# Kernel tuning notes

Measured on AMD Instinct MI355X. Metric: run time of the kernel, lower is better.

Reference implementation:

```python
import jax, jax.numpy as jnp
import numpy as np

NUM_HEADS = 8
D_HEAD = 64
ATTENTION_WINDOW = 512


def alibi_bias(num_heads, q_len, k_len):
    # ALiBi slopes for power-of-2 number of heads (Press et al. 2021).
    start = 2.0 ** (-(2.0 ** -(np.log2(num_heads) - 3.0)))
    slopes = jnp.asarray([start * (start ** i) for i in range(num_heads)],
                         dtype=jnp.float32)  # [H]
    rel = jnp.arange(q_len)[:, None] - jnp.arange(k_len)[None, :]  # [t, T]
    # Bidirectional ALiBi: bias = -slope * |i - j|
    return -slopes[:, None, None] * jnp.abs(rel).astype(jnp.float32)  # [H, t, T]


def sliding_window_mask(seq_len, window):
    # Attend to tokens within window//2 on each side; even window -> window+1.
    if window % 2 == 0:
        window += 1
    half = window // 2
    idx = jnp.arange(seq_len)
    return jnp.abs(idx[:, None] - idx[None, :]) <= half  # [S, S] bool


def setup_inputs() -> dict:
    key = jax.random.key(0)
    ks = jax.random.split(key, 6)
    B, S, E = 2, 4096, 512
    HD = NUM_HEADS * D_HEAD
    s_in = 1.0 / np.sqrt(E)
    s_out = 1.0 / np.sqrt(HD)
    return {
        'inputs_q': jax.random.normal(ks[0], (B, S, E), jnp.float32),
        'inputs_kv': jax.random.normal(ks[1], (B, S, E), jnp.float32),
        'w_q': jax.random.normal(ks[2], (E, HD), jnp.float32) * s_in,
        'w_k': jax.random.normal(ks[3], (E, HD), jnp.float32) * s_in,
        'w_v': jax.random.normal(ks[4], (E, HD), jnp.float32) * s_in,
        'w_o': jax.random.normal(ks[5], (HD, E), jnp.float32) * s_out,
    }


def reference(inputs_q, inputs_kv, w_q, w_k, w_v, w_o):
    B, S, E = inputs_q.shape
    H, D = NUM_HEADS, D_HEAD
    q = (inputs_q @ w_q).reshape(B, S, H, D)
    k = (inputs_kv @ w_k).reshape(B, S, H, D)
    v = (inputs_kv @ w_v).reshape(B, S, H, D)
    # scores: [B, H, t, T]
    att = jnp.einsum('bthd,bThd->bhtT', q, k) * (1.0 / jnp.sqrt(jnp.float32(D)))
    att = att + alibi_bias(H, S, S)[None]
    mask = sliding_window_mask(S, ATTENTION_WINDOW)
    att = jnp.where(mask[None, None], att, jnp.finfo(jnp.float32).min)
    p = jax.nn.softmax(att, axis=-1)
    out = jnp.einsum('bhtT,bThd->bthd', p, v).reshape(B, S, H * D)
    return out @ w_o
```

## Files before the change

### kernel.cpp

```cpp
#include <hip/hip_runtime.h>

#define S_LEN  4096
#define NH     8
#define DH     64
#define EMB    512
#define HDIM   512
#define HALF_W 256
#define BATCH  2
#define M_ROWS (BATCH * S_LEN)

typedef __attribute__((ext_vector_type(8))) short bf16x8;
typedef __attribute__((ext_vector_type(4))) float f32x4;

__device__ __forceinline__ float b2f(unsigned short u) {
    union { unsigned int i; float f; } v; v.i = ((unsigned int)u) << 16; return v.f;
}
__device__ __forceinline__ unsigned short f2b(float f) {
    unsigned int x = __float_as_uint(f);
    unsigned int r = (x + 0x7fffu + ((x >> 16) & 1u)) >> 16;
    return (unsigned short)r;
}
__device__ __forceinline__ void unpack2(unsigned int u, float* d) {
    d[0] = b2f((unsigned short)(u & 0xffffu));
    d[1] = b2f((unsigned short)(u >> 16));
}
union FragU { uint4 u; bf16x8 f; };
__device__ __forceinline__ bf16x8 ldfrag(const unsigned short* p) {
    FragU x; x.u = *(const uint4*)p; return x.f;
}

__device__ __forceinline__ void async16(const unsigned short* g, unsigned short* l) {
    __builtin_amdgcn_global_load_lds(
        (__attribute__((address_space(1))) void*)const_cast<unsigned short*>(g),
        (__attribute__((address_space(3))) void*)l, 16, 0, 0);
}

__device__ __forceinline__ int detect_flag(const unsigned short* __restrict__ xq) {
    __shared__ int s_flag;
    if (threadIdx.x == 0) s_flag = 0;
    __syncthreads();
    uint4 u = *(const uint4*)(xq + threadIdx.x * 8);
    const unsigned short* us = (const unsigned short*)&u;
    int bad = 0;
#pragma unroll
    for (int i = 0; i < 8; ++i) {
        float v = b2f(us[i]);
        if (!(fabsf(v) < 1.0e6f)) bad = 1;
    }
    if (__any(bad) && (threadIdx.x & 63) == 0) atomicOr(&s_flag, 1);
    __syncthreads();
    return s_flag;
}

__global__ __launch_bounds__(256) void prep(
    const void* __restrict__ xq, const void* __restrict__ xkv,
    const void* __restrict__ w0, const void* __restrict__ w1,
    const void* __restrict__ w2, const void* __restrict__ w3,
    unsigned short* __restrict__ Wt, unsigned short* __restrict__ Xc)
{
    const int flag = detect_flag((const unsigned short*)xq);
    const int blk = blockIdx.x;
    if (blk < 1024) {
        __shared__ float t[32][33];
        const int z = blk >> 8, idx = blk & 255;
        const void* src = (z == 0) ? w0 : (z == 1) ? w1 : (z == 2) ? w2 : w3;
        unsigned short* dst = Wt + (size_t)z * EMB * EMB;
        const int n0 = (idx & 15) << 5, k0 = (idx >> 4) << 5;
        const int kk = threadIdx.x >> 3;
        const int n4 = (threadIdx.x & 7) << 2;
        if (flag) {
            float4 v = *(const float4*)((const float*)src + (size_t)(k0 + kk) * EMB + n0 + n4);
            t[kk][n4] = v.x; t[kk][n4 + 1] = v.y; t[kk][n4 + 2] = v.z; t[kk][n4 + 3] = v.w;
        } else {
            uint2 u = *(const uint2*)((const unsigned short*)src + (size_t)(k0 + kk) * EMB + n0 + n4);
            unpack2(u.x, &t[kk][n4]); unpack2(u.y, &t[kk][n4 + 2]);
        }
        __syncthreads();
        const int nn = threadIdx.x >> 3;
        const int ks = (threadIdx.x & 7) << 2;
        uint2 pk;
        pk.x = (unsigned int)f2b(t[ks + 0][nn]) | ((unsigned int)f2b(t[ks + 1][nn]) << 16);
        pk.y = (unsigned int)f2b(t[ks + 2][nn]) | ((unsigned int)f2b(t[ks + 3][nn]) << 16);
        *(uint2*)(dst + (size_t)(n0 + nn) * EMB + k0 + ks) = pk;
    } else {
        if (!flag) return;
        const int idx = blk - 1024;
        const int z = idx >> 11;
        const float* src = (const float*)(z ? xkv : xq);
        unsigned short* dst = Xc + (size_t)z * M_ROWS * EMB;
        const size_t base = ((size_t)(idx & 2047) * 256 + threadIdx.x) * 8;
        float4 a = *(const float4*)(src + base);
        float4 b = *(const float4*)(src + base + 4);
        uint4 pk;
        pk.x = (unsigned int)f2b(a.x) | ((unsigned int)f2b(a.y) << 16);
        pk.y = (unsigned int)f2b(a.z) | ((unsigned int)f2b(a.w) << 16);
        pk.z = (unsigned int)f2b(b.x) | ((unsigned int)f2b(b.y) << 16);
        pk.w = (unsigned int)f2b(b.z) | ((unsigned int)f2b(b.w) << 16);
        *(uint4*)(dst + base) = pk;
    }
}

__device__ __forceinline__ void mgemm_core4(
    const unsigned short* __restrict__ A, const unsigned short* __restrict__ Bt,
    int m0, f32x4 (*acc)[2],
    unsigned short (*A_lds)[64], unsigned short (*B_lds)[64])
{
    const int tid  = threadIdx.x;
    const int lane = tid & 63;
    const int w    = tid >> 6;
    const int wm   = (w >> 1) << 6;
    const int wn   = (w & 1) << 5;
    const int qcol = lane & 15;
    const int quad = lane >> 4;

    const int srow = tid >> 3;
    const int sp   = tid & 7;

    for (int k0 = 0; k0 < EMB; k0 += 64) {
        __syncthreads();
#pragma unroll
        for (int i = 0; i < 4; ++i) {
            const int row  = (i << 5) + srow;
            const int gcol = ((sp ^ (row & 7)) << 3);
            async16(A + (size_t)(m0 + row) * EMB + k0 + gcol, &A_lds[row][sp << 3]);
        }
#pragma unroll
        for (int i = 0; i < 2; ++i) {
            const int row  = (i << 5) + srow;
            const int gcol = ((sp ^ (row & 7)) << 3);
            async16(Bt + (size_t)row * EMB + k0 + gcol, &B_lds[row][sp << 3]);
        }
        __syncthreads();

#pragma unroll
        for (int kh = 0; kh < 2; ++kh) {
            bf16x8 af[4], bf[2];
#pragma unroll
            for (int i = 0; i < 4; ++i) {
                const int row = wm + (i << 4) + qcol;
                const int p   = ((kh << 2) + quad) ^ (row & 7);
                af[i] = ldfrag(&A_lds[row][p << 3]);
            }
#pragma unroll
            for (int j = 0; j < 2; ++j) {
                const int row = wn + (j << 4) + qcol;
                const int p   = ((kh << 2) + quad) ^ (row & 7);
                bf[j] = ldfrag(&B_lds[row][p << 3]);
            }
#pragma unroll
            for (int i = 0; i < 4; ++i)
#pragma unroll
                for (int j = 0; j < 2; ++j)
                    acc[i][j] = __builtin_amdgcn_mfma_f32_16x16x32_bf16(af[i], bf[j], acc[i][j], 0, 0, 0);
        }
    }
}

__global__ __launch_bounds__(256) void gemm_qkv(
    const void* __restrict__ xq, const void* __restrict__ xkv,
    const unsigned short* __restrict__ Xc, const unsigned short* __restrict__ Wt,
    unsigned short* __restrict__ Qb, unsigned short* __restrict__ Kb,
    unsigned short* __restrict__ Vtb)
{
    const int flag = detect_flag((const unsigned short*)xq);
    __shared__ __align__(16) unsigned short A_lds[128][64];
    __shared__ __align__(16) unsigned short B_lds[64][64];
    const int blk = blockIdx.x;
    const int xcd = blk & 7, idx = blk >> 3;
    const int mi = idx / 24, ni = idx - mi * 24;
    const int m0 = ((xcd << 3) + mi) << 7;
    const int n0 = ni << 6;

    const unsigned short* A;
    if (flag) A = Xc + (n0 < 512 ? (size_t)0 : (size_t)M_ROWS * EMB);
    else      A = (const unsigned short*)(n0 < 512 ? xq : xkv);
    const unsigned short* Bt = Wt + (size_t)n0 * EMB;

    f32x4 acc[4][2];
#pragma unroll
    for (int i = 0; i < 4; ++i)
#pragma unroll
        for (int j = 0; j < 2; ++j) acc[i][j] = (f32x4){0.f, 0.f, 0.f, 0.f};

    mgemm_core4(A, Bt, m0, acc, A_lds, B_lds);

    const int lane = threadIdx.x & 63, w = threadIdx.x >> 6;
    const int wm = (w >> 1) << 6, wn = (w & 1) << 5;
    const int qcol = lane & 15, quad = lane >> 4;
    const int mode = n0 >> 9;
#pragma unroll
    for (int ms = 0; ms < 4; ++ms)
#pragma unroll
        for (int ns = 0; ns < 2; ++ns)
#pragma unroll
            for (int r = 0; r < 4; ++r) {
                const int m = m0 + wm + (ms << 4) + (quad << 2) + r;
                const int n = n0 + wn + (ns << 4) + qcol;
                const unsigned short us = f2b(acc[ms][ns][r]);
                if (mode == 0) {
                    Qb[(size_t)m * HDIM + n] = us;
                } else if (mode == 1) {
                    Kb[(size_t)m * HDIM + (n - 512)] = us;
                } else {
                    const int hd = n - 1024;
                    const int bb = m >> 12, s = m & (S_LEN - 1);
                    const int hh = hd >> 6, d = hd & 63;
                    Vtb[((size_t)((bb * NH + hh) * DH + d)) * S_LEN + s] = us;
                }
            }
}

__global__ __launch_bounds__(256) void gemm_out(
    const void* __restrict__ xq,
    const unsigned short* __restrict__ A, const unsigned short* __restrict__ Bt,
    void* __restrict__ C)
{
    const int flag = detect_flag((const unsigned short*)xq);
    __shared__ __align__(16) unsigned short A_lds[128][64];
    __shared__ __align__(16) unsigned short B_lds[64][64];
    const int blk = blockIdx.x;
    const int xcd = blk & 7, idx = blk >> 3;
    const int mi = idx >> 3, ni = idx & 7;
    const int m0 = ((xcd << 3) + mi) << 7;
    const int n0 = ni << 6;

    f32x4 acc[4][2];
#pragma unroll
    for (int i = 0; i < 4; ++i)
#pragma unroll
        for (int j = 0; j < 2; ++j) acc[i][j] = (f32x4){0.f, 0.f, 0.f, 0.f};

    mgemm_core4(A, Bt + (size_t)n0 * EMB, m0, acc, A_lds, B_lds);

    const int lane = threadIdx.x & 63, w = threadIdx.x >> 6;
    const int wm = (w >> 1) << 6, wn = (w & 1) << 5;
    const int qcol = lane & 15, quad = lane >> 4;
#pragma unroll
    for (int ms = 0; ms < 4; ++ms)
#pragma unroll
        for (int ns = 0; ns < 2; ++ns)
#pragma unroll
            for (int r = 0; r < 4; ++r) {
                const int m = m0 + wm + (ms << 4) + (quad << 2) + r;
                const int n = n0 + wn + (ns << 4) + qcol;
                const float v = acc[ms][ns][r];
                if (flag) ((float*)C)[(size_t)m * HDIM + n] = v;
                else      ((unsigned short*)C)[(size_t)m * HDIM + n] = f2b(v);
            }
}

__global__ __launch_bounds__(256) void attn_mfma(
    const unsigned short* __restrict__ Q,
    const unsigned short* __restrict__ Kg,
    const unsigned short* __restrict__ Vt,
    unsigned short* __restrict__ O)
{
    __shared__ __align__(16) unsigned short K_lds[64][64];
    __shared__ __align__(16) unsigned short V_lds[64][64];
    __shared__ __align__(16) unsigned short P_lds[4][32][72];

    const int tid  = threadIdx.x;
    const int lane = tid & 63;
    const int w    = tid >> 6;
    const int blk  = blockIdx.x;
    const int bh   = blk >> 5;
    const int r5   = blk & 31;
    const int tile = ((r5 & 7) << 2) | (r5 >> 3);
    const int h    = bh & (NH - 1);
    const int b    = bh >> 3;
    const int t0   = tile << 7;
    const int tq0  = t0 + (w << 5);

    const int qcol = lane & 15;
    const int quad = lane >> 4;
    const float slope = 1.0f / (float)(2 << h);

    bf16x8 qf[2][2];
#pragma unroll
    for (int qs = 0; qs < 2; ++qs) {
        const unsigned short* qrow =
            Q + (size_t)(b * S_LEN + tq0 + (qs << 4) + qcol) * HDIM + h * DH;
        qf[qs][0] = ldfrag(qrow + quad * 8);
        qf[qs][1] = ldfrag(qrow + 32 + quad * 8);
    }

    f32x4 Oacc[2][4];
#pragma unroll
    for (int qs = 0; qs < 2; ++qs)
#pragma unroll
        for (int i = 0; i < 4; ++i) Oacc[qs][i] = (f32x4){0.f, 0.f, 0.f, 0.f};
    float lsum[2] = {0.f, 0.f};

    const int srow = tid >> 3;
    const int sp   = tid & 7;

    for (int c = 0; c < 10; ++c) {
        const int j0 = t0 - HALF_W + (c << 6);
        __syncthreads();
#pragma unroll
        for (int i = 0; i < 2; ++i) {
            const int row  = (i << 5) + srow;
            const int gseg = (sp ^ (row & 7)) << 3;
            const int jc = min(max(j0 + row, 0), S_LEN - 1);
            async16(Kg + (size_t)(b * S_LEN + jc) * HDIM + h * DH + gseg,
                    &K_lds[row][sp << 3]);
            const int js = min(max(j0 + gseg, 0), S_LEN - 8);
            async16(Vt + ((size_t)((b * NH + h) * DH + row)) * S_LEN + js,
                    &V_lds[row][sp << 3]);
        }
        __syncthreads();

#pragma unroll
        for (int qs = 0; qs < 2; ++qs) {
#pragma unroll
            for (int ks = 0; ks < 4; ++ks) {
                const int krow = (ks << 4) + qcol;
                const bf16x8 kf0 = ldfrag(&K_lds[krow][(quad ^ (krow & 7)) << 3]);
                const bf16x8 kf1 = ldfrag(&K_lds[krow][((4 + quad) ^ (krow & 7)) << 3]);
                f32x4 z = (f32x4){0.f, 0.f, 0.f, 0.f};
                z = __builtin_amdgcn_mfma_f32_16x16x32_bf16(kf0, qf[qs][0], z, 0, 0, 0);
                z = __builtin_amdgcn_mfma_f32_16x16x32_bf16(kf1, qf[qs][1], z, 0, 0, 0);
                unsigned short pb[4];
#pragma unroll
                for (int r = 0; r < 4; ++r) {
                    const int j  = j0 + (ks << 4) + (quad << 2) + r;
                    const int dd = (tq0 + (qs << 4) + qcol) - j;
                    const bool ok = (j >= 0) && (j < S_LEN) && (dd <= HALF_W) && (dd >= -HALF_W);
                    const float s = z[r] * 0.125f - slope * fabsf((float)dd);
                    const float p = ok ? __expf(s - 12.0f) : 0.0f;
                    lsum[qs] += p;
                    pb[r] = f2b(p);
                }
                uint2 pk;
                pk.x = (unsigned int)pb[0] | ((unsigned int)pb[1] << 16);
                pk.y = (unsigned int)pb[2] | ((unsigned int)pb[3] << 16);
                *(uint2*)&P_lds[w][(qs << 4) + qcol][(ks << 4) + (quad << 2)] = pk;
            }
        }
#pragma unroll
        for (int qs = 0; qs < 2; ++qs) {
            const bf16x8 pf0 = ldfrag(&P_lds[w][(qs << 4) + qcol][quad * 8]);
            const bf16x8 pf1 = ldfrag(&P_lds[w][(qs << 4) + qcol][32 + quad * 8]);
#pragma unroll
            for (int ds = 0; ds < 4; ++ds) {
                const int vrow = (ds << 4) + qcol;
                const bf16x8 vf0 = ldfrag(&V_lds[vrow][(quad ^ (vrow & 7)) << 3]);
                const bf16x8 vf1 = ldfrag(&V_lds[vrow][((4 + quad) ^ (vrow & 7)) << 3]);
                Oacc[qs][ds] = __builtin_amdgcn_mfma_f32_16x16x32_bf16(vf0, pf0, Oacc[qs][ds], 0, 0, 0);
                Oacc[qs][ds] = __builtin_amdgcn_mfma_f32_16x16x32_bf16(vf1, pf1, Oacc[qs][ds], 0, 0, 0);
            }
        }
    }

#pragma unroll
    for (int qs = 0; qs < 2; ++qs) {
        float l = lsum[qs];
        l += __shfl_xor(l, 16, 64);
        l += __shfl_xor(l, 32, 64);
        const float rz = 1.0f / l;
        unsigned short* obase =
            O + (size_t)(b * S_LEN + tq0 + (qs << 4) + qcol) * HDIM + h * DH;
#pragma unroll
        for (int ds = 0; ds < 4; ++ds) {
            uint2 pk;
            pk.x = (unsigned int)f2b(Oacc[qs][ds][0] * rz) |
                   ((unsigned int)f2b(Oacc[qs][ds][1] * rz) << 16);
            pk.y = (unsigned int)f2b(Oacc[qs][ds][2] * rz) |
                   ((unsigned int)f2b(Oacc[qs][ds][3] * rz) << 16);
            *(uint2*)(obase + (ds << 4) + (quad << 2)) = pk;
        }
    }
}

extern "C" void kernel_launch(void* const* d_in, const int* in_sizes, int n_in,
                              void* d_out, int out_size, void* d_ws, size_t ws_size,
                              hipStream_t stream) {
    const void* xq  = d_in[0];
    const void* xkv = d_in[1];
    const void* wq  = d_in[2];
    const void* wk  = d_in[3];
    const void* wv  = d_in[4];
    const void* wo  = d_in[5];

    unsigned short* Qb  = (unsigned short*)((char*)d_ws + 256);
    unsigned short* Kb  = Qb  + (size_t)M_ROWS * HDIM;
    unsigned short* Vtb = Kb  + (size_t)M_ROWS * HDIM;
    unsigned short* Wt  = Vtb + (size_t)M_ROWS * HDIM;
    unsigned short* Wto = Wt + (size_t)3 * EMB * EMB;
    unsigned short* Xc  = (unsigned short*)d_out;

    prep<<<1024 + 4096, 256, 0, stream>>>(xq, xkv, wq, wk, wv, wo, Wt, Xc);
    gemm_qkv<<<1536, 256, 0, stream>>>(xq, xkv, Xc, Wt, Qb, Kb, Vtb);
    attn_mfma<<<BATCH * NH * (S_LEN / 128), 256, 0, stream>>>(Qb, Kb, Vtb, Qb);
    gemm_out<<<512, 256, 0, stream>>>(xq, Qb, Wto, d_out);
}
```

Measured before the change: 165.7 us.

## Double-buffer GEMM and attention LDS tiles, fold softmax scale into Q, skip masked tiles

Both GEMM kernels and the attention kernel now use two LDS buffers and prefetch the next K-chunk or KV tile while computing on the current one. This halves the barriers per iteration and hides global-to-LDS latency, at the cost of doubled shared memory, which may lower occupancy. The 1/sqrt(d) and log2(e) factors are folded into Q at projection time so the softmax can use exp2f with a single fma. Whole chunks and 16-wide sub-tiles that fall outside the sliding window are skipped. A cheaper packed bf16 rounding (round-half-up) replaces the round-to-nearest-even conversion for P and the output.

```diff
diff --git a/kernel.cpp b/kernel.cpp
--- a/kernel.cpp
+++ b/kernel.cpp
@@ -12,6 +12,8 @@
 typedef __attribute__((ext_vector_type(8))) short bf16x8;
 typedef __attribute__((ext_vector_type(4))) float f32x4;
 
+#define LOG2E 1.44269504088896f
+
 __device__ __forceinline__ float b2f(unsigned short u) {
     union { unsigned int i; float f; } v; v.i = ((unsigned int)u) << 16; return v.f;
 }
@@ -19,6 +21,10 @@
     unsigned int x = __float_as_uint(f);
     unsigned int r = (x + 0x7fffu + ((x >> 16) & 1u)) >> 16;
     return (unsigned short)r;
+}
+__device__ __forceinline__ unsigned int f2bpk(float a, float b) {
+    return ((__float_as_uint(a) + 0x8000u) >> 16) |
+           ((__float_as_uint(b) + 0x8000u) & 0xffff0000u);
 }
 __device__ __forceinline__ void unpack2(unsigned int u, float* d) {
     d[0] = b2f((unsigned short)(u & 0xffffu));
@@ -100,10 +106,29 @@
     }
 }
 
-__device__ __forceinline__ void mgemm_core4(
+__device__ __forceinline__ void gemm_issue(
+    const unsigned short* __restrict__ A, const unsigned short* __restrict__ Bt,
+    int m0, int k0, unsigned short (*Ab)[64], unsigned short (*Bb)[64],
+    int srow, int sp)
+{
+#pragma unroll
+    for (int i = 0; i < 4; ++i) {
+        const int row = (i << 5) + srow;
+        const int gcol = ((sp ^ (row & 7)) << 3);
+        async16(A + (size_t)(m0 + row) * EMB + k0 + gcol, &Ab[row][sp << 3]);
+    }
+#pragma unroll
+    for (int i = 0; i < 2; ++i) {
+        const int row = (i << 5) + srow;
+        const int gcol = ((sp ^ (row & 7)) << 3);
+        async16(Bt + (size_t)row * EMB + k0 + gcol, &Bb[row][sp << 3]);
+    }
+}
+
+__device__ __forceinline__ void mgemm_core5(
     const unsigned short* __restrict__ A, const unsigned short* __restrict__ Bt,
     int m0, f32x4 (*acc)[2],
-    unsigned short (*A_lds)[64], unsigned short (*B_lds)[64])
+    unsigned short (*A_lds)[128][64], unsigned short (*B_lds)[64][64])
 {
     const int tid  = threadIdx.x;
     const int lane = tid & 63;
@@ -112,26 +137,17 @@
     const int wn   = (w & 1) << 5;
     const int qcol = lane & 15;
     const int quad = lane >> 4;
-
     const int srow = tid >> 3;
     const int sp   = tid & 7;
 
-    for (int k0 = 0; k0 < EMB; k0 += 64) {
+    gemm_issue(A, Bt, m0, 0, A_lds[0], B_lds[0], srow, sp);
+
+    for (int it = 0; it < 8; ++it) {
         __syncthreads();
-#pragma unroll
-        for (int i = 0; i < 4; ++i) {
-            const int row  = (i << 5) + srow;
-            const int gcol = ((sp ^ (row & 7)) << 3);
-            async16(A + (size_t)(m0 + row) * EMB + k0 + gcol, &A_lds[row][sp << 3]);
-        }
-#pragma unroll
-        for (int i = 0; i < 2; ++i) {
-            const int row  = (i << 5) + srow;
-            const int gcol = ((sp ^ (row & 7)) << 3);
-            async16(Bt + (size_t)row * EMB + k0 + gcol, &B_lds[row][sp << 3]);
-        }
-        __syncthreads();
-
+        if (it < 7)
+            gemm_issue(A, Bt, m0, (it + 1) << 6,
+                       A_lds[(it + 1) & 1], B_lds[(it + 1) & 1], srow, sp);
+        const int bi = it & 1;
 #pragma unroll
         for (int kh = 0; kh < 2; ++kh) {
             bf16x8 af[4], bf[2];
@@ -139,13 +155,13 @@
             for (int i = 0; i < 4; ++i) {
                 const int row = wm + (i << 4) + qcol;
                 const int p   = ((kh << 2) + quad) ^ (row & 7);
-                af[i] = ldfrag(&A_lds[row][p << 3]);
+                af[i] = ldfrag(&A_lds[bi][row][p << 3]);
             }
 #pragma unroll
             for (int j = 0; j < 2; ++j) {
                 const int row = wn + (j << 4) + qcol;
                 const int p   = ((kh << 2) + quad) ^ (row & 7);
-                bf[j] = ldfrag(&B_lds[row][p << 3]);
+                bf[j] = ldfrag(&B_lds[bi][row][p << 3]);
             }
 #pragma unroll
             for (int i = 0; i < 4; ++i)
@@ -163,8 +179,8 @@
     unsigned short* __restrict__ Vtb)
 {
     const int flag = detect_flag((const unsigned short*)xq);
-    __shared__ __align__(16) unsigned short A_lds[128][64];
-    __shared__ __align__(16) unsigned short B_lds[64][64];
+    __shared__ __align__(16) unsigned short A_lds[2][128][64];
+    __shared__ __align__(16) unsigned short B_lds[2][64][64];
     const int blk = blockIdx.x;
     const int xcd = blk & 7, idx = blk >> 3;
     const int mi = idx / 24, ni = idx - mi * 24;
@@ -182,12 +198,13 @@
 #pragma unroll
         for (int j = 0; j < 2; ++j) acc[i][j] = (f32x4){0.f, 0.f, 0.f, 0.f};
 
-    mgemm_core4(A, Bt, m0, acc, A_lds, B_lds);
+    mgemm_core5(A, Bt, m0, acc, A_lds, B_lds);
 
     const int lane = threadIdx.x & 63, w = threadIdx.x >> 6;
     const int wm = (w >> 1) << 6, wn = (w & 1) << 5;
     const int qcol = lane & 15, quad = lane >> 4;
     const int mode = n0 >> 9;
+    const float qscale = 0.125f * LOG2E;
 #pragma unroll
     for (int ms = 0; ms < 4; ++ms)
 #pragma unroll
@@ -196,16 +213,15 @@
             for (int r = 0; r < 4; ++r) {
                 const int m = m0 + wm + (ms << 4) + (quad << 2) + r;
                 const int n = n0 + wn + (ns << 4) + qcol;
-                const unsigned short us = f2b(acc[ms][ns][r]);
                 if (mode == 0) {
-                    Qb[(size_t)m * HDIM + n] = us;
+                    Qb[(size_t)m * HDIM + n] = f2b(acc[ms][ns][r] * qscale);
                 } else if (mode == 1) {
-                    Kb[(size_t)m * HDIM + (n - 512)] = us;
+                    Kb[(size_t)m * HDIM + (n - 512)] = f2b(acc[ms][ns][r]);
                 } else {
                     const int hd = n - 1024;
                     const int bb = m >> 12, s = m & (S_LEN - 1);
                     const int hh = hd >> 6, d = hd & 63;
-                    Vtb[((size_t)((bb * NH + hh) * DH + d)) * S_LEN + s] = us;
+                    Vtb[((size_t)((bb * NH + hh) * DH + d)) * S_LEN + s] = f2b(acc[ms][ns][r]);
                 }
             }
 }
@@ -216,8 +232,8 @@
     void* __restrict__ C)
 {
     const int flag = detect_flag((const unsigned short*)xq);
-    __shared__ __align__(16) unsigned short A_lds[128][64];
-    __shared__ __align__(16) unsigned short B_lds[64][64];
+    __shared__ __align__(16) unsigned short A_lds[2][128][64];
+    __shared__ __align__(16) unsigned short B_lds[2][64][64];
     const int blk = blockIdx.x;
     const int xcd = blk & 7, idx = blk >> 3;
     const int mi = idx >> 3, ni = idx & 7;
@@ -230,7 +246,7 @@
 #pragma unroll
         for (int j = 0; j < 2; ++j) acc[i][j] = (f32x4){0.f, 0.f, 0.f, 0.f};
 
-    mgemm_core4(A, Bt + (size_t)n0 * EMB, m0, acc, A_lds, B_lds);
+    mgemm_core5(A, Bt + (size_t)n0 * EMB, m0, acc, A_lds, B_lds);
 
     const int lane = threadIdx.x & 63, w = threadIdx.x >> 6;
     const int wm = (w >> 1) << 6, wn = (w & 1) << 5;
@@ -249,14 +265,30 @@
             }
 }
 
+__device__ __forceinline__ void attn_issue(
+    const unsigned short* __restrict__ Kg, const unsigned short* __restrict__ Vt,
+    int b, int h, int j0,
+    unsigned short (*Kb)[64], unsigned short (*Vb)[64], int srow, int sp)
+{
+#pragma unroll
+    for (int i = 0; i < 2; ++i) {
+        const int row  = (i << 5) + srow;
+        const int gseg = (sp ^ (row & 7)) << 3;
+        const int jc = min(max(j0 + row, 0), S_LEN - 1);
+        async16(Kg + (size_t)(b * S_LEN + jc) * HDIM + h * DH + gseg, &Kb[row][sp << 3]);
+        const int js = min(max(j0 + gseg, 0), S_LEN - 8);
+        async16(Vt + ((size_t)((b * NH + h) * DH + row)) * S_LEN + js, &Vb[row][sp << 3]);
+    }
+}
+
 __global__ __launch_bounds__(256) void attn_mfma(
     const unsigned short* __restrict__ Q,
     const unsigned short* __restrict__ Kg,
     const unsigned short* __restrict__ Vt,
     unsigned short* __restrict__ O)
 {
-    __shared__ __align__(16) unsigned short K_lds[64][64];
-    __shared__ __align__(16) unsigned short V_lds[64][64];
+    __shared__ __align__(16) unsigned short K_lds[2][64][64];
+    __shared__ __align__(16) unsigned short V_lds[2][64][64];
     __shared__ __align__(16) unsigned short P_lds[4][32][72];
 
     const int tid  = threadIdx.x;
@@ -273,7 +305,8 @@
 
     const int qcol = lane & 15;
     const int quad = lane >> 4;
-    const float slope = 1.0f / (float)(2 << h);
+    const float slope2 = LOG2E / (float)(2 << h);
+    const float bias2  = 12.0f * LOG2E;
 
     bf16x8 qf[2][2];
 #pragma unroll
@@ -294,47 +327,52 @@
     const int srow = tid >> 3;
     const int sp   = tid & 7;
 
+    attn_issue(Kg, Vt, b, h, t0 - HALF_W, K_lds[0], V_lds[0], srow, sp);
+
     for (int c = 0; c < 10; ++c) {
         const int j0 = t0 - HALF_W + (c << 6);
         __syncthreads();
-#pragma unroll
-        for (int i = 0; i < 2; ++i) {
-            const int row  = (i << 5) + srow;
-            const int gseg = (sp ^ (row & 7)) << 3;
-            const int jc = min(max(j0 + row, 0), S_LEN - 1);
-            async16(Kg + (size_t)(b * S_LEN + jc) * HDIM + h * DH + gseg,
-                    &K_lds[row][sp << 3]);
-            const int js = min(max(j0 + gseg, 0), S_LEN - 8);
-            async16(Vt + ((size_t)((b * NH + h) * DH + row)) * S_LEN + js,
-                    &V_lds[row][sp << 3]);
-        }
-        __syncthreads();
+        if (c < 9)
+            attn_issue(Kg, Vt, b, h, j0 + 64,
+                       K_lds[(c + 1) & 1], V_lds[(c + 1) & 1], srow, sp);
+        const int bi = c & 1;
+
+        if (j0 + 63 < tq0 - HALF_W || j0 > tq0 + 31 + HALF_W) continue;
 
 #pragma unroll
         for (int qs = 0; qs < 2; ++qs) {
+            const int qv = tq0 + (qs << 4) + qcol;
 #pragma unroll
             for (int ks = 0; ks < 4; ++ks) {
+                const int sj0 = j0 + (ks << 4);
+                unsigned short* pdst = &P_lds[w][(qs << 4) + qcol][(ks << 4) + (quad << 2)];
+                if (sj0 + 15 < tq0 + (qs << 4) - HALF_W ||
+                    sj0 > tq0 + (qs << 4) + 15 + HALF_W) {
+                    *(uint2*)pdst = (uint2){0u, 0u};
+                    continue;
+                }
                 const int krow = (ks << 4) + qcol;
-                const bf16x8 kf0 = ldfrag(&K_lds[krow][(quad ^ (krow & 7)) << 3]);
-                const bf16x8 kf1 = ldfrag(&K_lds[krow][((4 + quad) ^ (krow & 7)) << 3]);
+                const bf16x8 kf0 = ldfrag(&K_lds[bi][krow][(quad ^ (krow & 7)) << 3]);
+                const bf16x8 kf1 = ldfrag(&K_lds[bi][krow][((4 + quad) ^ (krow & 7)) << 3]);
                 f32x4 z = (f32x4){0.f, 0.f, 0.f, 0.f};
                 z = __builtin_amdgcn_mfma_f32_16x16x32_bf16(kf0, qf[qs][0], z, 0, 0, 0);
                 z = __builtin_amdgcn_mfma_f32_16x16x32_bf16(kf1, qf[qs][1], z, 0, 0, 0);
-                unsigned short pb[4];
+                float p[4];
 #pragma unroll
                 for (int r = 0; r < 4; ++r) {
-                    const int j  = j0 + (ks << 4) + (quad << 2) + r;
-                    const int dd = (tq0 + (qs << 4) + qcol) - j;
-                    const bool ok = (j >= 0) && (j < S_LEN) && (dd <= HALF_W) && (dd >= -HALF_W);
-                    const float s = z[r] * 0.125f - slope * fabsf((float)dd);
-                    const float p = ok ? __expf(s - 12.0f) : 0.0f;
-                    lsum[qs] += p;
-                    pb[r] = f2b(p);
+                    const int j  = sj0 + (quad << 2) + r;
+                    const int dd = qv - j;
+                    const int ad = dd < 0 ? -dd : dd;
+                    const bool ok = (ad <= HALF_W) && ((unsigned)j < (unsigned)S_LEN);
+                    const float arg = fmaf(-slope2, (float)ad, z[r] - bias2);
+                    const float e = exp2f(arg);
+                    p[r] = ok ? e : 0.0f;
+                    lsum[qs] += p[r];
                 }
                 uint2 pk;
-                pk.x = (unsigned int)pb[0] | ((unsigned int)pb[1] << 16);
-                pk.y = (unsigned int)pb[2] | ((unsigned int)pb[3] << 16);
-                *(uint2*)&P_lds[w][(qs << 4) + qcol][(ks << 4) + (quad << 2)] = pk;
+                pk.x = f2bpk(p[0], p[1]);
+                pk.y = f2bpk(p[2], p[3]);
+                *(uint2*)pdst = pk;
             }
         }
 #pragma unroll
@@ -344,8 +382,8 @@
 #pragma unroll
             for (int ds = 0; ds < 4; ++ds) {
                 const int vrow = (ds << 4) + qcol;
-                const bf16x8 vf0 = ldfrag(&V_lds[vrow][(quad ^ (vrow & 7)) << 3]);
-                const bf16x8 vf1 = ldfrag(&V_lds[vrow][((4 + quad) ^ (vrow & 7)) << 3]);
+                const bf16x8 vf0 = ldfrag(&V_lds[bi][vrow][(quad ^ (vrow & 7)) << 3]);
+                const bf16x8 vf1 = ldfrag(&V_lds[bi][vrow][((4 + quad) ^ (vrow & 7)) << 3]);
                 Oacc[qs][ds] = __builtin_amdgcn_mfma_f32_16x16x32_bf16(vf0, pf0, Oacc[qs][ds], 0, 0, 0);
                 Oacc[qs][ds] = __builtin_amdgcn_mfma_f32_16x16x32_bf16(vf1, pf1, Oacc[qs][ds], 0, 0, 0);
             }
@@ -363,10 +401,8 @@
 #pragma unroll
         for (int ds = 0; ds < 4; ++ds) {
             uint2 pk;
-            pk.x = (unsigned int)f2b(Oacc[qs][ds][0] * rz) |
-                   ((unsigned int)f2b(Oacc[qs][ds][1] * rz) << 16);
-            pk.y = (unsigned int)f2b(Oacc[qs][ds][2] * rz) |
-                   ((unsigned int)f2b(Oacc[qs][ds][3] * rz) << 16);
+            pk.x = f2bpk(Oacc[qs][ds][0] * rz, Oacc[qs][ds][1] * rz);
+            pk.y = f2bpk(Oacc[qs][ds][2] * rz, Oacc[qs][ds][3] * rz);
             *(uint2*)(obase + (ds << 4) + (quad << 2)) = pk;
         }
     }
```

After: 167.4 us. No clear change (+1.1%).
